# Kernel tuning notes

Measured on AMD Instinct MI355X. Metric: run time of the kernel, lower is better.

Reference implementation:

```python
import jax, jax.numpy as jnp
import numpy as np
from jax import lax

B, FIN, FOUT, K, H, W = 4, 64, 64, 3, 128, 128


def setup_inputs() -> dict:
    key = jax.random.key(0)
    k1, k2, k3, k4, k5 = jax.random.split(key, 5)
    # fan-out per-channel conv weights: one KxK kernel per (out, in) pair
    fan = 1.0 / np.sqrt(K * K)  # torch Conv2d(1,1,K) init scale
    Wf = jax.random.uniform(k1, (FOUT, FIN, K, K), jnp.float32, -fan, fan)
    bf = jax.random.uniform(k2, (FOUT, FIN), jnp.float32, -fan, fan)
    # 1x1 combine: Conv2d(FIN, 1, 1) per output channel
    fc = 1.0 / np.sqrt(FIN)
    Wc = jax.random.uniform(k3, (FOUT, FIN), jnp.float32, -fc, fc)
    bc = jax.random.uniform(k4, (FOUT,), jnp.float32, -fc, fc)
    x = jax.random.normal(k5, (B, FIN, H, W), jnp.float32)
    return {"x": x, "Wf": Wf, "bf": bf, "Wc": Wc, "bc": bc}


def reference(x, Wf, bf, Wc, bc):
    fout, fin, k, _ = Wf.shape
    # Depthwise conv with channel multiplier fout: group i (input channel i)
    # produces output channels i*fout .. i*fout+fout-1, i.e. pair (i, o).
    kern = jnp.transpose(Wf, (2, 3, 1, 0)).reshape(k, k, 1, fin * fout)  # HWIO
    y = lax.conv_general_dilated(
        x, kern, window_strides=(1, 1), padding='VALID',
        dimension_numbers=('NCHW', 'HWIO', 'NCHW'),
        feature_group_count=fin)  # [B, fin*fout, H', W']
    y = y + bf.T.reshape(1, fin * fout, 1, 1)  # bias for pair (i, o)
    y = jax.nn.relu(y)
    b, _, h2, w2 = y.shape
    y = y.reshape(b, fin, fout, h2, w2)
    # 1x1 combine: out[b,o] = sum_i Wc[o,i] * y[b,i,o] + bc[o]
    out = jnp.einsum('biohw,oi->bohw', y, Wc) + bc[None, :, None, None]
    return out
```

## Files before the change

### kernel.cpp

```cpp
#include <hip/hip_runtime.h>

typedef _Float16 f16;
typedef f16 f16x4 __attribute__((ext_vector_type(4)));
typedef f16 f16x8 __attribute__((ext_vector_type(8)));
typedef float f32x4 __attribute__((ext_vector_type(4)));
typedef float f32x16 __attribute__((ext_vector_type(16)));
typedef unsigned int uint32;

#define FIN  64
#define FOUT 64
#define HI   128
#define WI   128
#define HO   126
#define WO   126
#define HIWI (HI*WI)
#define NPH  16
#define CPH  4
#define TR   8
#define TC   16
#define SR   10
#define SDW  12
#define NUNIT (CPH*SR*5)


__global__ __launch_bounds__(256) void prepass(
    const float* __restrict__ Wf, const float* __restrict__ bf,
    unsigned short* __restrict__ ws)
{
    int t = blockIdx.x * 256 + threadIdx.x;
    int i  = t >> 7;
    int ob = (t >> 6) & 1;
    int l  = t & 63;
    int g  = l >> 5, n = l & 31;
    int o  = ob * 32 + n;
    unsigned short h[8];
#pragma unroll
    for (int j = 0; j < 8; ++j) {
        int k = g * 4 + (j & 3) + 8 * (j >> 2);
        float v = 0.0f;
        if (k < 12) {
            int dy = k >> 2, dx = k & 3;
            if (dx < 3) v = Wf[((size_t)o * FIN + i) * 9 + dy * 3 + dx];
        } else if (k == 12) {
            v = bf[o * FIN + i];
        }
        f16 hv = (f16)v;
        h[j] = *(unsigned short*)&hv;
    }
    uint4 pk;
    pk.x = h[0] | ((uint32)h[1] << 16);
    pk.y = h[2] | ((uint32)h[3] << 16);
    pk.z = h[4] | ((uint32)h[5] << 16);
    pk.w = h[6] | ((uint32)h[7] << 16);
    *(uint4*)&ws[(size_t)t * 8] = pk;
}

__global__ __launch_bounds__(256, 4) void conv_mfma(
    const float* __restrict__ x,  const float* __restrict__ Wc,
    const float* __restrict__ bc, const unsigned short* __restrict__ ws,
    float* __restrict__ out)
{
    __shared__ __align__(16) union {
        struct { uint32 xsl[2][CPH * SR * SDW]; float wcl[32][68]; } a;
        float ot[32][132];
    } sm;

    const int tid = threadIdx.x;
    const int l   = tid & 63, w = tid >> 6;
    const int g   = l >> 5;
    const int m   = l & 31;
    const int prow = m >> 2;
    const int sx   = w * 4 + (m & 3);

    const int fid    = blockIdx.x;
    const int grp    = (fid >> 7) * 8 + (fid & 7);
    const int member = (fid >> 3) & 15;
    const int rx = grp & 15, b = grp >> 4;
    const int cy = member & 7, oh = member >> 3;
    const int row0 = rx * TR;
    const int col0 = cy * TC;
    const int o_lane = oh * 32 + m;

#pragma unroll
    for (int k = 0; k < 8; ++k) {
        int idx = tid + k * 256;
        sm.a.wcl[idx >> 6][idx & 63] =
            Wc[(size_t)(oh * 32 + (idx >> 6)) * FIN + (idx & 63)];
    }

    const float* xb = x + (size_t)b * FIN * HIWI;
    const bool stg = (tid < NUNIT);
    int uch = 0, goff = 0, widx = 0;
    if (stg) {
        uch = tid / 50;
        int rem = tid % 50;
        int r = rem / 5, u = rem % 5;
        int gy = min(row0 + r, HI - 1);
        int gx = min(col0 + 4 * u, WI - 4);
        goff = gy * WI + gx;
        widx = (uch * SR + r) * SDW + 2 * u;
    }

    if (stg) {
        f32x4 v = *(const f32x4*)&xb[(size_t)uch * HIWI + goff];
        f16x4 h; h[0] = (f16)v[0]; h[1] = (f16)v[1]; h[2] = (f16)v[2]; h[3] = (f16)v[3];
        *(uint2*)&sm.a.xsl[0][widx] = *(uint2*)&h;
    }

    const uint4* Btab = (const uint4*)ws;
    uint4 Bc[CPH], Bn[CPH];
#pragma unroll
    for (int ch = 0; ch < CPH; ++ch)
        Bc[ch] = Btab[(size_t)(ch * 2 + oh) * 64 + l];

    f32x16 acc = {}, zero = {};
    const bool odd = (sx & 1);
    const int  qd  = sx >> 1;

    for (int ph = 0; ph < NPH; ++ph) {
        const int cur = ph & 1;
        const bool more = (ph + 1 < NPH);

        f32x4 sv = {};
        if (more) {
            const int ib = (ph + 1) * CPH;
            if (stg) sv = *(const f32x4*)&xb[(size_t)(ib + uch) * HIWI + goff];
#pragma unroll
            for (int ch = 0; ch < CPH; ++ch)
                Bn[ch] = Btab[(size_t)((ib + ch) * 2 + oh) * 64 + l];
        }

        __syncthreads();

        const f32x4 wcq = *(const f32x4*)&sm.a.wcl[m][ph * CPH];

#pragma unroll
        for (int ch = 0; ch < CPH; ++ch) {
            const uint32* rp1 = &sm.a.xsl[cur][(ch * SR + prow + g) * SDW];
            const uint32* rp2 = &sm.a.xsl[cur][(ch * SR + prow + 2) * SDW];
            uint32 d0 = rp1[qd], d1 = rp1[qd + 1];
            uint32 e0 = rp2[qd], e1 = rp2[qd + 1];
            uint32 a0 = odd ? ((d0 >> 16) | (d1 << 16)) : d0;
            uint32 a1 = odd ? (d1 >> 16) : d1;
            uint32 b0 = odd ? ((e0 >> 16) | (e1 << 16)) : e0;
            uint32 b1 = odd ? (e1 >> 16) : e1;
            if (g) { b0 = 0x00003c00u; b1 = 0u; }
            uint4 auv = {a0, a1, b0, b1};
            f16x8 Af = *(f16x8*)&auv;
            f16x8 Bf = *(f16x8*)&Bc[ch];
            f32x16 S = __builtin_amdgcn_mfma_f32_32x32x16_f16(Af, Bf, zero, 0, 0, 0);
            const float wcv = wcq[ch];
#pragma unroll
            for (int r = 0; r < 16; ++r)
                acc[r] = fmaf(wcv, fmaxf(S[r], 0.0f), acc[r]);
        }

        if (more) {
            if (stg) {
                f16x4 h; h[0] = (f16)sv[0]; h[1] = (f16)sv[1];
                h[2] = (f16)sv[2]; h[3] = (f16)sv[3];
                *(uint2*)&sm.a.xsl[cur ^ 1][widx] = *(uint2*)&h;
            }
#pragma unroll
            for (int ch = 0; ch < CPH; ++ch) Bc[ch] = Bn[ch];
        }
    }

    __syncthreads();

    const float bcv = bc[o_lane];
#pragma unroll
    for (int r = 0; r < 16; ++r) {
        int p  = (r & 3) + 8 * (r >> 2) + 4 * g;
        int px = (p >> 2) * TC + w * 4 + (p & 3);
        sm.ot[m][px] = acc[r] + bcv;
    }
    __syncthreads();

    {
        const int oo  = tid >> 3;
        const int seg = tid & 7;
        const int o   = oh * 32 + oo;
        const int ho  = row0 + seg;
        if (ho < HO) {
            const float* src = &sm.ot[oo][seg * TC];
            size_t base = ((size_t)(b * FOUT + o) * HO + ho) * WO + col0;
            const int nst = (col0 + TC <= WO) ? TC : (WO - col0);
            for (int c = 0; c < nst; ++c) out[base + c] = src[c];
        }
    }
}

extern "C" void kernel_launch(void* const* d_in, const int* in_sizes, int n_in,
                              void* d_out, int out_size, void* d_ws, size_t ws_size,
                              hipStream_t stream) {
    const float* x  = (const float*)d_in[0];
    const float* Wf = (const float*)d_in[1];
    const float* bf = (const float*)d_in[2];
    const float* Wc = (const float*)d_in[3];
    const float* bc = (const float*)d_in[4];
    float* out = (float*)d_out;
    unsigned short* ws = (unsigned short*)d_ws;

    hipLaunchKernelGGL(prepass, dim3(32), dim3(256), 0, stream, Wf, bf, ws);

    hipLaunchKernelGGL(conv_mfma, dim3(1024), dim3(256), 0, stream,
                       x, Wc, bc, ws, out);
}
```

Baseline: 48.37 us.

## Split input-channel reduction across two wave groups with 512-thread blocks

Doubles the block to 512 threads. Two groups of four waves each handle half of the 64 input channels (32 apiece), which halves the serial phase loop from 16 to 8. Each phase now stages 8 channel slices into shared memory, and the two groups' partial accumulators are summed through a shared-memory buffer before the bias-add and store epilogue. This aims to expose more parallel waves and reduce serial latency per block, at the cost of extra LDS, an additional reduction step with syncs, and higher per-block resource use that may cut occupancy.

After: 46.74 us. 3.4% less time.

```diff
diff --git a/kernel.cpp b/kernel.cpp
--- a/kernel.cpp
+++ b/kernel.cpp
@@ -14,13 +14,15 @@
 #define HO   126
 #define WO   126
 #define HIWI (HI*WI)
-#define NPH  16
-#define CPH  4
+#define NPH  8
 #define TR   8
 #define TC   16
 #define SR   10
 #define SDW  12
-#define NUNIT (CPH*SR*5)
+#define CHSTR (SR*SDW)
+#define NSLOT 8
+#define XBUF (NSLOT*CHSTR)
+#define NUNIT 400
 
 
 __global__ __launch_bounds__(256) void prepass(
@@ -55,22 +57,28 @@
     *(uint4*)&ws[(size_t)t * 8] = pk;
 }
 
-__global__ __launch_bounds__(256, 4) void conv_mfma(
+__global__ __launch_bounds__(512, 4) void conv_mfma(
     const float* __restrict__ x,  const float* __restrict__ Wc,
     const float* __restrict__ bc, const unsigned short* __restrict__ ws,
     float* __restrict__ out)
 {
     __shared__ __align__(16) union {
-        struct { uint32 xsl[2][CPH * SR * SDW]; float wcl[32][68]; } a;
+        struct { uint32 xsl[2][XBUF]; float wcl[32][68]; } a;
+        float part[4][64][16];
         float ot[32][132];
     } sm;
 
     const int tid = threadIdx.x;
     const int l   = tid & 63, w = tid >> 6;
+    const int wg  = w >> 2;
+    const int wl  = w & 3;
     const int g   = l >> 5;
     const int m   = l & 31;
     const int prow = m >> 2;
-    const int sx   = w * 4 + (m & 3);
+    const int sx   = wl * 4 + (m & 3);
+    const bool odd = (sx & 1);
+    const int  qd  = sx >> 1;
+    const int ibase = wg * 32;
 
     const int fid    = blockIdx.x;
     const int grp    = (fid >> 7) * 8 + (fid & 7);
@@ -82,40 +90,39 @@
     const int o_lane = oh * 32 + m;
 
 #pragma unroll
-    for (int k = 0; k < 8; ++k) {
-        int idx = tid + k * 256;
+    for (int k = 0; k < 4; ++k) {
+        int idx = tid + k * 512;
         sm.a.wcl[idx >> 6][idx & 63] =
             Wc[(size_t)(oh * 32 + (idx >> 6)) * FIN + (idx & 63)];
     }
 
     const float* xb = x + (size_t)b * FIN * HIWI;
     const bool stg = (tid < NUNIT);
-    int uch = 0, goff = 0, widx = 0;
+    int slot = 0, goff = 0, widx = 0;
     if (stg) {
-        uch = tid / 50;
+        slot = tid / 50;
         int rem = tid % 50;
         int r = rem / 5, u = rem % 5;
         int gy = min(row0 + r, HI - 1);
         int gx = min(col0 + 4 * u, WI - 4);
         goff = gy * WI + gx;
-        widx = (uch * SR + r) * SDW + 2 * u;
-    }
+        widx = slot * CHSTR + r * SDW + 2 * u;
+    }
+    const int chbase = (slot >> 2) * 32 + (slot & 3);
 
     if (stg) {
-        f32x4 v = *(const f32x4*)&xb[(size_t)uch * HIWI + goff];
+        f32x4 v = *(const f32x4*)&xb[(size_t)chbase * HIWI + goff];
         f16x4 h; h[0] = (f16)v[0]; h[1] = (f16)v[1]; h[2] = (f16)v[2]; h[3] = (f16)v[3];
         *(uint2*)&sm.a.xsl[0][widx] = *(uint2*)&h;
     }
 
     const uint4* Btab = (const uint4*)ws;
-    uint4 Bc[CPH], Bn[CPH];
-#pragma unroll
-    for (int ch = 0; ch < CPH; ++ch)
-        Bc[ch] = Btab[(size_t)(ch * 2 + oh) * 64 + l];
+    uint4 Bc[4], Bn[4];
+#pragma unroll
+    for (int c4 = 0; c4 < 4; ++c4)
+        Bc[c4] = Btab[(size_t)((ibase + c4) * 2 + oh) * 64 + l];
 
     f32x16 acc = {}, zero = {};
-    const bool odd = (sx & 1);
-    const int  qd  = sx >> 1;
 
     for (int ph = 0; ph < NPH; ++ph) {
         const int cur = ph & 1;
@@ -123,23 +130,24 @@
 
         f32x4 sv = {};
         if (more) {
-            const int ib = (ph + 1) * CPH;
-            if (stg) sv = *(const f32x4*)&xb[(size_t)(ib + uch) * HIWI + goff];
-#pragma unroll
-            for (int ch = 0; ch < CPH; ++ch)
-                Bn[ch] = Btab[(size_t)((ib + ch) * 2 + oh) * 64 + l];
+            if (stg) sv = *(const f32x4*)
+                &xb[(size_t)(chbase + (ph + 1) * 4) * HIWI + goff];
+#pragma unroll
+            for (int c4 = 0; c4 < 4; ++c4)
+                Bn[c4] = Btab[(size_t)((ibase + (ph + 1) * 4 + c4) * 2 + oh) * 64 + l];
         }
 
         __syncthreads();
 
-        const f32x4 wcq = *(const f32x4*)&sm.a.wcl[m][ph * CPH];
-
-#pragma unroll
-        for (int ch = 0; ch < CPH; ++ch) {
-            const uint32* rp1 = &sm.a.xsl[cur][(ch * SR + prow + g) * SDW];
-            const uint32* rp2 = &sm.a.xsl[cur][(ch * SR + prow + 2) * SDW];
-            uint32 d0 = rp1[qd], d1 = rp1[qd + 1];
-            uint32 e0 = rp2[qd], e1 = rp2[qd + 1];
+        const f32x4 wcq = *(const f32x4*)&sm.a.wcl[m][ibase + ph * 4];
+        const uint32* base = sm.a.xsl[cur];
+
+#pragma unroll
+        for (int c4 = 0; c4 < 4; ++c4) {
+            const uint32* r1 = base + (wg * 4 + c4) * CHSTR + (prow + g) * SDW;
+            const uint32* r2 = base + (wg * 4 + c4) * CHSTR + (prow + 2) * SDW;
+            uint32 d0 = r1[qd], d1 = r1[qd + 1];
+            uint32 e0 = r2[qd], e1 = r2[qd + 1];
             uint32 a0 = odd ? ((d0 >> 16) | (d1 << 16)) : d0;
             uint32 a1 = odd ? (d1 >> 16) : d1;
             uint32 b0 = odd ? ((e0 >> 16) | (e1 << 16)) : e0;
@@ -147,9 +155,9 @@
             if (g) { b0 = 0x00003c00u; b1 = 0u; }
             uint4 auv = {a0, a1, b0, b1};
             f16x8 Af = *(f16x8*)&auv;
-            f16x8 Bf = *(f16x8*)&Bc[ch];
+            f16x8 Bf = *(f16x8*)&Bc[c4];
             f32x16 S = __builtin_amdgcn_mfma_f32_32x32x16_f16(Af, Bf, zero, 0, 0, 0);
-            const float wcv = wcq[ch];
+            const float wcv = wcq[c4];
 #pragma unroll
             for (int r = 0; r < 16; ++r)
                 acc[r] = fmaf(wcv, fmaxf(S[r], 0.0f), acc[r]);
@@ -162,22 +170,34 @@
                 *(uint2*)&sm.a.xsl[cur ^ 1][widx] = *(uint2*)&h;
             }
 #pragma unroll
-            for (int ch = 0; ch < CPH; ++ch) Bc[ch] = Bn[ch];
-        }
-    }
-
-    __syncthreads();
-
-    const float bcv = bc[o_lane];
-#pragma unroll
-    for (int r = 0; r < 16; ++r) {
-        int p  = (r & 3) + 8 * (r >> 2) + 4 * g;
-        int px = (p >> 2) * TC + w * 4 + (p & 3);
-        sm.ot[m][px] = acc[r] + bcv;
-    }
-    __syncthreads();
-
-    {
+            for (int c4 = 0; c4 < 4; ++c4) Bc[c4] = Bn[c4];
+        }
+    }
+
+    __syncthreads();
+    if (wg == 1) {
+#pragma unroll
+        for (int r = 0; r < 16; ++r) sm.part[wl][l][r] = acc[r];
+    }
+    __syncthreads();
+    if (wg == 0) {
+#pragma unroll
+        for (int r = 0; r < 16; ++r) acc[r] += sm.part[wl][l][r];
+    }
+    __syncthreads();
+
+    if (wg == 0) {
+        const float bcv = bc[o_lane];
+#pragma unroll
+        for (int r = 0; r < 16; ++r) {
+            int p  = (r & 3) + 8 * (r >> 2) + 4 * g;
+            int px = (p >> 2) * TC + wl * 4 + (p & 3);
+            sm.ot[m][px] = acc[r] + bcv;
+        }
+    }
+    __syncthreads();
+
+    if (tid < 256) {
         const int oo  = tid >> 3;
         const int seg = tid & 7;
         const int o   = oh * 32 + oo;
@@ -204,6 +224,6 @@
 
     hipLaunchKernelGGL(prepass, dim3(32), dim3(256), 0, stream, Wf, bf, ws);
 
-    hipLaunchKernelGGL(conv_mfma, dim3(1024), dim3(256), 0, stream,
+    hipLaunchKernelGGL(conv_mfma, dim3(1024), dim3(512), 0, stream,
                        x, Wc, bc, ws, out);
 }
```

## Load conv inputs directly into registers and combine channel pairs with fdot2

Applied to the files above, without the earlier changes.

Removes the LDS double-buffered staging of x. Each lane now loads its own 3x3 patch elements straight from global memory, two input channels at a time, with a register-level prefetch of the next pair, and the per-phase __syncthreads barriers go away. Wc is pre-packed to fp16 pairs in the prepass. The ReLU-and-combine step now packs two channels' MFMA results to fp16 and accumulates them with v_dot2, which halves the VALU work per channel but rounds the activations to fp16. The cost is many redundant, uncoalesced scalar global loads that rely on cache, and the output store loop is specialized so it can be unrolled.

Result: faster. 40.48 us (-16.3%).

```diff
diff --git a/kernel.cpp b/kernel.cpp
--- a/kernel.cpp
+++ b/kernel.cpp
@@ -1,9 +1,8 @@
 #include <hip/hip_runtime.h>
 
 typedef _Float16 f16;
-typedef f16 f16x4 __attribute__((ext_vector_type(4)));
+typedef __fp16 h2 __attribute__((ext_vector_type(2)));
 typedef f16 f16x8 __attribute__((ext_vector_type(8)));
-typedef float f32x4 __attribute__((ext_vector_type(4)));
 typedef float f32x16 __attribute__((ext_vector_type(16)));
 typedef unsigned int uint32;
 
@@ -14,63 +13,88 @@
 #define HO   126
 #define WO   126
 #define HIWI (HI*WI)
-#define NPH  16
-#define CPH  4
 #define TR   8
 #define TC   16
-#define SR   10
-#define SDW  12
-#define NUNIT (CPH*SR*5)
 
 
 __global__ __launch_bounds__(256) void prepass(
     const float* __restrict__ Wf, const float* __restrict__ bf,
-    unsigned short* __restrict__ ws)
+    const float* __restrict__ Wc, unsigned short* __restrict__ ws)
 {
     int t = blockIdx.x * 256 + threadIdx.x;
-    int i  = t >> 7;
-    int ob = (t >> 6) & 1;
-    int l  = t & 63;
-    int g  = l >> 5, n = l & 31;
-    int o  = ob * 32 + n;
-    unsigned short h[8];
-#pragma unroll
-    for (int j = 0; j < 8; ++j) {
-        int k = g * 4 + (j & 3) + 8 * (j >> 2);
-        float v = 0.0f;
-        if (k < 12) {
-            int dy = k >> 2, dx = k & 3;
-            if (dx < 3) v = Wf[((size_t)o * FIN + i) * 9 + dy * 3 + dx];
-        } else if (k == 12) {
-            v = bf[o * FIN + i];
-        }
-        f16 hv = (f16)v;
-        h[j] = *(unsigned short*)&hv;
-    }
-    uint4 pk;
-    pk.x = h[0] | ((uint32)h[1] << 16);
-    pk.y = h[2] | ((uint32)h[3] << 16);
-    pk.z = h[4] | ((uint32)h[5] << 16);
-    pk.w = h[6] | ((uint32)h[7] << 16);
-    *(uint4*)&ws[(size_t)t * 8] = pk;
+    if (t < 8192) {
+        int i  = t >> 7;
+        int ob = (t >> 6) & 1;
+        int l  = t & 63;
+        int g  = l >> 5, n = l & 31;
+        int o  = ob * 32 + n;
+        unsigned short h[8];
+#pragma unroll
+        for (int j = 0; j < 8; ++j) {
+            int k = g * 4 + (j & 3) + 8 * (j >> 2);
+            float v = 0.0f;
+            if (k < 12) {
+                int dy = k >> 2, dx = k & 3;
+                if (dx < 3) v = Wf[((size_t)o * FIN + i) * 9 + dy * 3 + dx];
+            } else if (k == 12) {
+                v = bf[o * FIN + i];
+            }
+            f16 hv = (f16)v;
+            h[j] = *(unsigned short*)&hv;
+        }
+        uint4 pk;
+        pk.x = h[0] | ((uint32)h[1] << 16);
+        pk.y = h[2] | ((uint32)h[3] << 16);
+        pk.z = h[4] | ((uint32)h[5] << 16);
+        pk.w = h[6] | ((uint32)h[7] << 16);
+        *(uint4*)&ws[(size_t)t * 8] = pk;
+    } else if (t < 8192 + 2048) {
+        int t2 = t - 8192;
+        int ip = t2 >> 6, o = t2 & 63;
+        f16 lo = (f16)Wc[(size_t)o * FIN + 2 * ip];
+        f16 hi = (f16)Wc[(size_t)o * FIN + 2 * ip + 1];
+        uint32 v = (uint32)*(unsigned short*)&lo |
+                   ((uint32)*(unsigned short*)&hi << 16);
+        ((uint32*)ws)[32768 + t2] = v;
+    }
+}
+
+struct PR {
+    float a10, a11, a12, a20, a21, a22;
+    float b10, b11, b12, b20, b21, b22;
+    uint4 aB, bB;
+    uint32 wcu;
+};
+
+__device__ __forceinline__ PR loadPair(const float* xb, const uint4* Btab,
+                                       const uint32* wct, int ip,
+                                       int goff1, int goff2, int oh, int l,
+                                       int o_lane)
+{
+    PR r;
+    const float* xa = xb + (size_t)(2 * ip) * HIWI;
+    const float* xc = xa + HIWI;
+    r.a10 = xa[goff1]; r.a11 = xa[goff1 + 1]; r.a12 = xa[goff1 + 2];
+    r.a20 = xa[goff2]; r.a21 = xa[goff2 + 1]; r.a22 = xa[goff2 + 2];
+    r.b10 = xc[goff1]; r.b11 = xc[goff1 + 1]; r.b12 = xc[goff1 + 2];
+    r.b20 = xc[goff2]; r.b21 = xc[goff2 + 1]; r.b22 = xc[goff2 + 2];
+    r.aB = Btab[(size_t)((2 * ip) * 2 + oh) * 64 + l];
+    r.bB = Btab[(size_t)((2 * ip + 1) * 2 + oh) * 64 + l];
+    r.wcu = wct[ip * 64 + o_lane];
+    return r;
 }
 
 __global__ __launch_bounds__(256, 4) void conv_mfma(
-    const float* __restrict__ x,  const float* __restrict__ Wc,
-    const float* __restrict__ bc, const unsigned short* __restrict__ ws,
-    float* __restrict__ out)
+    const float* __restrict__ x,  const float* __restrict__ bc,
+    const unsigned short* __restrict__ ws, float* __restrict__ out)
 {
-    __shared__ __align__(16) union {
-        struct { uint32 xsl[2][CPH * SR * SDW]; float wcl[32][68]; } a;
-        float ot[32][132];
-    } sm;
+    __shared__ float ot[32][132];
 
     const int tid = threadIdx.x;
     const int l   = tid & 63, w = tid >> 6;
     const int g   = l >> 5;
     const int m   = l & 31;
     const int prow = m >> 2;
-    const int sx   = w * 4 + (m & 3);
 
     const int fid    = blockIdx.x;
     const int grp    = (fid >> 7) * 8 + (fid & 7);
@@ -81,99 +105,97 @@
     const int col0 = cy * TC;
     const int o_lane = oh * 32 + m;
 
-#pragma unroll
-    for (int k = 0; k < 8; ++k) {
-        int idx = tid + k * 256;
-        sm.a.wcl[idx >> 6][idx & 63] =
-            Wc[(size_t)(oh * 32 + (idx >> 6)) * FIN + (idx & 63)];
-    }
-
-    const float* xb = x + (size_t)b * FIN * HIWI;
-    const bool stg = (tid < NUNIT);
-    int uch = 0, goff = 0, widx = 0;
-    if (stg) {
-        uch = tid / 50;
-        int rem = tid % 50;
-        int r = rem / 5, u = rem % 5;
-        int gy = min(row0 + r, HI - 1);
-        int gx = min(col0 + 4 * u, WI - 4);
-        goff = gy * WI + gx;
-        widx = (uch * SR + r) * SDW + 2 * u;
-    }
-
-    if (stg) {
-        f32x4 v = *(const f32x4*)&xb[(size_t)uch * HIWI + goff];
-        f16x4 h; h[0] = (f16)v[0]; h[1] = (f16)v[1]; h[2] = (f16)v[2]; h[3] = (f16)v[3];
-        *(uint2*)&sm.a.xsl[0][widx] = *(uint2*)&h;
-    }
-
-    const uint4* Btab = (const uint4*)ws;
-    uint4 Bc[CPH], Bn[CPH];
-#pragma unroll
-    for (int ch = 0; ch < CPH; ++ch)
-        Bc[ch] = Btab[(size_t)(ch * 2 + oh) * 64 + l];
-
-    f32x16 acc = {}, zero = {};
-    const bool odd = (sx & 1);
-    const int  qd  = sx >> 1;
-
-    for (int ph = 0; ph < NPH; ++ph) {
-        const int cur = ph & 1;
-        const bool more = (ph + 1 < NPH);
-
-        f32x4 sv = {};
-        if (more) {
-            const int ib = (ph + 1) * CPH;
-            if (stg) sv = *(const f32x4*)&xb[(size_t)(ib + uch) * HIWI + goff];
-#pragma unroll
-            for (int ch = 0; ch < CPH; ++ch)
-                Bn[ch] = Btab[(size_t)((ib + ch) * 2 + oh) * 64 + l];
-        }
-
-        __syncthreads();
-
-        const f32x4 wcq = *(const f32x4*)&sm.a.wcl[m][ph * CPH];
-
-#pragma unroll
-        for (int ch = 0; ch < CPH; ++ch) {
-            const uint32* rp1 = &sm.a.xsl[cur][(ch * SR + prow + g) * SDW];
-            const uint32* rp2 = &sm.a.xsl[cur][(ch * SR + prow + 2) * SDW];
-            uint32 d0 = rp1[qd], d1 = rp1[qd + 1];
-            uint32 e0 = rp2[qd], e1 = rp2[qd + 1];
-            uint32 a0 = odd ? ((d0 >> 16) | (d1 << 16)) : d0;
-            uint32 a1 = odd ? (d1 >> 16) : d1;
-            uint32 b0 = odd ? ((e0 >> 16) | (e1 << 16)) : e0;
-            uint32 b1 = odd ? (e1 >> 16) : e1;
-            if (g) { b0 = 0x00003c00u; b1 = 0u; }
-            uint4 auv = {a0, a1, b0, b1};
-            f16x8 Af = *(f16x8*)&auv;
-            f16x8 Bf = *(f16x8*)&Bc[ch];
-            f32x16 S = __builtin_amdgcn_mfma_f32_32x32x16_f16(Af, Bf, zero, 0, 0, 0);
-            const float wcv = wcq[ch];
-#pragma unroll
-            for (int r = 0; r < 16; ++r)
-                acc[r] = fmaf(wcv, fmaxf(S[r], 0.0f), acc[r]);
-        }
-
-        if (more) {
-            if (stg) {
-                f16x4 h; h[0] = (f16)sv[0]; h[1] = (f16)sv[1];
-                h[2] = (f16)sv[2]; h[3] = (f16)sv[3];
-                *(uint2*)&sm.a.xsl[cur ^ 1][widx] = *(uint2*)&h;
+    const int gy1 = min(row0 + prow + g, HI - 1);
+    const int gy2 = min(row0 + prow + 2, HI - 1);
+    const int cc  = min(col0 + w * 4 + (m & 3), WI - 3);
+    const int goff1 = gy1 * WI + cc;
+    const int goff2 = gy2 * WI + cc;
+
+    const float*  xb   = x + (size_t)b * FIN * HIWI;
+    const uint4*  Btab = (const uint4*)ws;
+    const uint32* wct  = ((const uint32*)ws) + 32768;
+
+    f32x16 acc = {};
+    const f32x16 zero = {};
+    const h2 zh = {(__fp16)0.0f, (__fp16)0.0f};
+
+    PR cur = loadPair(xb, Btab, wct, 0, goff1, goff2, oh, l, o_lane);
+
+#pragma unroll 4
+    for (int ip = 0; ip < 31; ++ip) {
+        PR nxt = loadPair(xb, Btab, wct, ip + 1, goff1, goff2, oh, l, o_lane);
+
+        {
+            uint32 a0 = __builtin_bit_cast(uint32, __builtin_amdgcn_cvt_pkrtz(cur.a10, cur.a11));
+            uint32 a1 = __builtin_bit_cast(uint32, __builtin_amdgcn_cvt_pkrtz(cur.a12, cur.a12));
+            uint32 a2 = g ? 0x00003c00u
+                          : __builtin_bit_cast(uint32, __builtin_amdgcn_cvt_pkrtz(cur.a20, cur.a21));
+            uint32 a3 = g ? 0u
+                          : __builtin_bit_cast(uint32, __builtin_amdgcn_cvt_pkrtz(cur.a22, cur.a22));
+            uint4 av = {a0, a1, a2, a3};
+            f32x16 S0 = __builtin_amdgcn_mfma_f32_32x32x16_f16(
+                __builtin_bit_cast(f16x8, av), __builtin_bit_cast(f16x8, cur.aB),
+                zero, 0, 0, 0);
+
+            uint32 b0 = __builtin_bit_cast(uint32, __builtin_amdgcn_cvt_pkrtz(cur.b10, cur.b11));
+            uint32 b1 = __builtin_bit_cast(uint32, __builtin_amdgcn_cvt_pkrtz(cur.b12, cur.b12));
+            uint32 b2 = g ? 0x00003c00u
+                          : __builtin_bit_cast(uint32, __builtin_amdgcn_cvt_pkrtz(cur.b20, cur.b21));
+            uint32 b3 = g ? 0u
+                          : __builtin_bit_cast(uint32, __builtin_amdgcn_cvt_pkrtz(cur.b22, cur.b22));
+            uint4 bv = {b0, b1, b2, b3};
+            f32x16 S1 = __builtin_amdgcn_mfma_f32_32x32x16_f16(
+                __builtin_bit_cast(f16x8, bv), __builtin_bit_cast(f16x8, cur.bB),
+                zero, 0, 0, 0);
+
+            h2 wch = __builtin_bit_cast(h2, cur.wcu);
+#pragma unroll
+            for (int r = 0; r < 16; ++r) {
+                h2 q = __builtin_amdgcn_cvt_pkrtz(S0[r], S1[r]);
+                q = __builtin_elementwise_max(q, zh);
+                acc[r] = __builtin_amdgcn_fdot2(q, wch, acc[r], false);
             }
-#pragma unroll
-            for (int ch = 0; ch < CPH; ++ch) Bc[ch] = Bn[ch];
-        }
-    }
-
-    __syncthreads();
+        }
+        cur = nxt;
+    }
+    {
+        uint32 a0 = __builtin_bit_cast(uint32, __builtin_amdgcn_cvt_pkrtz(cur.a10, cur.a11));
+        uint32 a1 = __builtin_bit_cast(uint32, __builtin_amdgcn_cvt_pkrtz(cur.a12, cur.a12));
+        uint32 a2 = g ? 0x00003c00u
+                      : __builtin_bit_cast(uint32, __builtin_amdgcn_cvt_pkrtz(cur.a20, cur.a21));
+        uint32 a3 = g ? 0u
+                      : __builtin_bit_cast(uint32, __builtin_amdgcn_cvt_pkrtz(cur.a22, cur.a22));
+        uint4 av = {a0, a1, a2, a3};
+        f32x16 S0 = __builtin_amdgcn_mfma_f32_32x32x16_f16(
+            __builtin_bit_cast(f16x8, av), __builtin_bit_cast(f16x8, cur.aB),
+            zero, 0, 0, 0);
+
+        uint32 b0 = __builtin_bit_cast(uint32, __builtin_amdgcn_cvt_pkrtz(cur.b10, cur.b11));
+        uint32 b1 = __builtin_bit_cast(uint32, __builtin_amdgcn_cvt_pkrtz(cur.b12, cur.b12));
+        uint32 b2 = g ? 0x00003c00u
+                      : __builtin_bit_cast(uint32, __builtin_amdgcn_cvt_pkrtz(cur.b20, cur.b21));
+        uint32 b3 = g ? 0u
+                      : __builtin_bit_cast(uint32, __builtin_amdgcn_cvt_pkrtz(cur.b22, cur.b22));
+        uint4 bv = {b0, b1, b2, b3};
+        f32x16 S1 = __builtin_amdgcn_mfma_f32_32x32x16_f16(
+            __builtin_bit_cast(f16x8, bv), __builtin_bit_cast(f16x8, cur.bB),
+            zero, 0, 0, 0);
+
+        h2 wch = __builtin_bit_cast(h2, cur.wcu);
+#pragma unroll
+        for (int r = 0; r < 16; ++r) {
+            h2 q = __builtin_amdgcn_cvt_pkrtz(S0[r], S1[r]);
+            q = __builtin_elementwise_max(q, zh);
+            acc[r] = __builtin_amdgcn_fdot2(q, wch, acc[r], false);
+        }
+    }
 
     const float bcv = bc[o_lane];
 #pragma unroll
     for (int r = 0; r < 16; ++r) {
         int p  = (r & 3) + 8 * (r >> 2) + 4 * g;
         int px = (p >> 2) * TC + w * 4 + (p & 3);
-        sm.ot[m][px] = acc[r] + bcv;
+        ot[m][px] = acc[r] + bcv;
     }
     __syncthreads();
 
@@ -183,10 +205,15 @@
         const int o   = oh * 32 + oo;
         const int ho  = row0 + seg;
         if (ho < HO) {
-            const float* src = &sm.ot[oo][seg * TC];
+            const float* src = &ot[oo][seg * TC];
             size_t base = ((size_t)(b * FOUT + o) * HO + ho) * WO + col0;
-            const int nst = (col0 + TC <= WO) ? TC : (WO - col0);
-            for (int c = 0; c < nst; ++c) out[base + c] = src[c];
+            if (col0 + TC <= WO) {
+#pragma unroll
+                for (int c = 0; c < TC; ++c) out[base + c] = src[c];
+            } else {
+#pragma unroll
+                for (int c = 0; c < 14; ++c) out[base + c] = src[c];
+            }
         }
     }
 }
@@ -202,8 +229,8 @@
     float* out = (float*)d_out;
     unsigned short* ws = (unsigned short*)d_ws;
 
-    hipLaunchKernelGGL(prepass, dim3(32), dim3(256), 0, stream, Wf, bf, ws);
+    hipLaunchKernelGGL(prepass, dim3(40), dim3(256), 0, stream, Wf, bf, Wc, ws);
 
     hipLaunchKernelGGL(conv_mfma, dim3(1024), dim3(256), 0, stream,
-                       x, Wc, bc, ws, out);
-}
+                       x, bc, ws, out);
+}
```
